# Kernel optimization log

Measured on AMD Instinct MI355X. Metric: run time of the kernel, lower is better.

## Reference

```python
import jax, jax.numpy as jnp
import numpy as np

M, K, D = 64, 32, 32   # antennas, users, hidden features
PT = 1.0               # total transmit power
BS = 1024


def _glorot(key, shape):
    fan_out, fan_in = shape
    lim = np.sqrt(6.0 / (fan_in + fan_out)).astype(np.float32)
    return jax.random.uniform(key, shape, minval=-lim, maxval=lim, dtype=jnp.float32)


def setup_inputs() -> dict:
    key = jax.random.key(0)
    ks = jax.random.split(key, 16)
    inp = {"x": jax.random.normal(ks[0], (BS, M, K, 2), dtype=jnp.float32)}
    dims = [(D, 2), (D, D), (D, D), (D, D), (2, D)]
    i = 1
    for l, sh in enumerate(dims, start=1):
        for tag in ("s", "m", "k"):
            inp[f"W{l}{tag}"] = _glorot(ks[i], sh)
            i += 1
    return inp


def gnn_layer(x, Ws, Wm, Wk):
    # x: (b, M, K, d_in); weights: (d_out, d_in)
    msg_m = jnp.sum(x, axis=2)  # (b, M, d_in) aggregate over users per antenna
    msg_k = jnp.sum(x, axis=1)  # (b, K, d_in) aggregate over antennas per user
    z = (jnp.einsum('hd,bmkd->bmkh', Ws, x)
         + jnp.einsum('hd,bmd->bmh', Wm, msg_m)[:, :, None, :]
         + jnp.einsum('hd,bkd->bkh', Wk, msg_k)[:, None, :, :])
    return z  # (b, M, K, d_out)


def pwr_norm(x):
    # x: (b, M, K, 2) -> |W|_F^2 = sum over m,k of re^2+im^2
    power = jnp.sum(x * x, axis=(1, 2, 3), keepdims=True)
    alpha = jnp.sqrt(PT / power)
    return alpha * x


def reference(x, W1s, W1m, W1k, W2s, W2m, W2k, W3s, W3m, W3k,
              W4s, W4m, W4k, W5s, W5m, W5k):
    h = jax.nn.relu(gnn_layer(x, W1s, W1m, W1k))
    h = jax.nn.relu(gnn_layer(h, W2s, W2m, W2k))
    h = jax.nn.relu(gnn_layer(h, W3s, W3m, W3k))
    h = jax.nn.relu(gnn_layer(h, W4s, W4m, W4k))
    h = gnn_layer(h, W5s, W5m, W5k)
    return pwr_norm(h)
```

## Files before the change

kernel.cpp:

```cpp
#include <hip/hip_runtime.h>
#include <hip/hip_fp16.h>


namespace {

constexpr int NTHREADS = 1024;
constexpr float INPUT_SCALE = 0.0625f;
constexpr float LAYER_SCALE = 0.0078125f;

typedef _Float16 half8 __attribute__((ext_vector_type(8)));
typedef _Float16 half2v __attribute__((ext_vector_type(2)));
typedef float    f32x4 __attribute__((ext_vector_type(4)));
typedef unsigned uint4v __attribute__((ext_vector_type(4)));

#define RPT32(X) X(0)X(1)X(2)X(3)X(4)X(5)X(6)X(7)X(8)X(9)X(10)X(11)X(12)X(13)X(14)X(15) \
                 X(16)X(17)X(18)X(19)X(20)X(21)X(22)X(23)X(24)X(25)X(26)X(27)X(28)X(29)X(30)X(31)
#define RPT16P(X) X(0,0,1)X(1,2,3)X(2,4,5)X(3,6,7)X(4,8,9)X(5,10,11)X(6,12,13)X(7,14,15) \
                  X(8,16,17)X(9,18,19)X(10,20,21)X(11,22,23)X(12,24,25)X(13,26,27)X(14,28,29)X(15,30,31)

#define AB_OFF(h) ((((h) >> 2) & 3) * 8 + (((h) >> 4) & 1) * 4 + ((h) & 3))
#define PSLOT(s) (2 * ((s) >> 2) + 8 * (((s) >> 1) & 1) + ((s) & 1))

__device__ __forceinline__ float2 upk(unsigned w) {
    __half2 h;
    *reinterpret_cast<unsigned*>(&h) = w;
    return __half22float2(h);
}
__device__ __forceinline__ unsigned pkz(float a, float b) {
    auto h = __builtin_amdgcn_cvt_pkrtz(a, b);
    return __builtin_bit_cast(unsigned, h);
}
__device__ __forceinline__ unsigned hadd2u(unsigned a, unsigned b) {
    half2v x = __builtin_bit_cast(half2v, a);
    half2v y = __builtin_bit_cast(half2v, b);
    return __builtin_bit_cast(unsigned, x + y);
}
__device__ __forceinline__ unsigned hmax0u(unsigned a) {
    unsigned r;
    asm("v_pk_max_f16 %0, %1, 0" : "=v"(r) : "v"(a));
    return r;
}
template <int CTRL>
__device__ __forceinline__ uint4v dpp_hadd(uint4v s) {
    uint4v r;
    r.x = hadd2u(s.x, (unsigned)__builtin_amdgcn_mov_dpp((int)s.x, CTRL, 0xF, 0xF, true));
    r.y = hadd2u(s.y, (unsigned)__builtin_amdgcn_mov_dpp((int)s.y, CTRL, 0xF, 0xF, true));
    r.z = hadd2u(s.z, (unsigned)__builtin_amdgcn_mov_dpp((int)s.z, CTRL, 0xF, 0xF, true));
    r.w = hadd2u(s.w, (unsigned)__builtin_amdgcn_mov_dpp((int)s.w, CTRL, 0xF, 0xF, true));
    return r;
}

__device__ __forceinline__ half8 load_wfrag(const float* __restrict__ W, int h, int quad,
                                            float scale) {
    const float4 w0 = *reinterpret_cast<const float4*>(W + h * 32 + quad * 4);
    const float4 w1 = *reinterpret_cast<const float4*>(W + h * 32 + 16 + quad * 4);
    half8 b;
    b[0] = (_Float16)(w0.x * scale); b[1] = (_Float16)(w0.y * scale);
    b[2] = (_Float16)(w0.z * scale); b[3] = (_Float16)(w0.w * scale);
    b[4] = (_Float16)(w1.x * scale); b[5] = (_Float16)(w1.y * scale);
    b[6] = (_Float16)(w1.z * scale); b[7] = (_Float16)(w1.w * scale);
    return b;
}

__device__ __forceinline__ void phase_msg(const unsigned* __restrict__ Xs,
                                          unsigned* __restrict__ MSG, int t) {
    const int l = t & 63, w = t >> 6;
    {
        const int k3 = l & 7;
        const int k = ((w & 3) << 3) | k3;
        const int chunk = w >> 2;
        const int mo = l >> 3;
        const int chunkp = chunk ^ ((k3 >> 1) & 3);
        const unsigned* p = Xs + mo * 4096 + k * 16 + chunkp * 4;
        half8 acc{};
#pragma unroll
        for (int j = 0; j < 8; ++j)
            acc += __builtin_bit_cast(half8, *(const uint4v*)(p + j * 512));
        uint4v s = __builtin_bit_cast(uint4v, acc);
        s = dpp_hadd<0x128>(s);
        if ((l & 8) == 0) {
            const int qi = l >> 4;
            *(uint4v*)(MSG + (128 + qi * 32 + k) * 20 + chunk * 4) = s;
        }
    }
    {
        const int k3 = l & 7;
        const int chunk = (l >> 3) & 3;
        const int mlow = ((l >> 5) & 1) | ((w & 15) << 1);
        const int chunkp = chunk ^ ((k3 >> 1) & 3);
        const unsigned* p = Xs + mlow * 512 + k3 * 16 + chunkp * 4;
        half8 accA{}, accB{};
#pragma unroll
        for (int j = 0; j < 4; ++j) {
            accA += __builtin_bit_cast(half8, *(const uint4v*)(p + j * 128));
            accB += __builtin_bit_cast(half8, *(const uint4v*)(p + 16384 + j * 128));
        }
        uint4v sA = __builtin_bit_cast(uint4v, accA);
        uint4v sB = __builtin_bit_cast(uint4v, accB);
        sA = dpp_hadd<0xB1>(sA); sA = dpp_hadd<0x4E>(sA);
        sB = dpp_hadd<0xB1>(sB); sB = dpp_hadd<0x4E>(sB);
        if ((l & 3) == 0) {
            const int set = (l >> 2) & 1;
            *(uint4v*)(MSG + (mlow + set * 64) * 20 + chunk * 4) = sA;
            *(uint4v*)(MSG + (mlow + 32 + set * 64) * 20 + chunk * 4) = sB;
        }
    }
}

__device__ __forceinline__ void phase_small(const float* __restrict__ Wmg,
                                            const float* __restrict__ Wkg,
                                            const unsigned* __restrict__ MSG,
                                            unsigned* __restrict__ ABu, int t) {
    const int w = t >> 6, lane = t & 63;
    if (w < 12) {
        const int isb = (w >= 8);
        const int ww = isb ? (w - 8) : w;
        const int nt = ww >> 1, ht = ww & 1;
        const int quad = lane >> 4, col = lane & 15;
        const half8 afrag = load_wfrag(isb ? Wkg : Wmg, ht * 16 + col, quad, LAYER_SCALE);
        f32x4 c = {0.f, 0.f, 0.f, 0.f};
        if (isb) {
            const int r0 = 128 + nt * 16 + col;
#pragma unroll
            for (int s = 0; s < 4; ++s) {
                const half8 bf = __builtin_bit_cast(half8,
                    *(const uint4v*)(MSG + (r0 + s * 32) * 20 + quad * 4));
                c = __builtin_amdgcn_mfma_f32_16x16x32_f16(afrag, bf, c, 0, 0, 0);
            }
        } else {
            const int r0 = nt * 16 + col;
#pragma unroll
            for (int s = 0; s < 2; ++s) {
                const half8 bf = __builtin_bit_cast(half8,
                    *(const uint4v*)(MSG + (r0 + s * 64) * 20 + quad * 4));
                c = __builtin_amdgcn_mfma_f32_16x16x32_f16(afrag, bf, c, 0, 0, 0);
            }
        }
        uint2 st;
        st.x = pkz(c[0], c[1]);
        st.y = pkz(c[2], c[3]);
        const int abrow = (isb ? 64 : 0) + nt * 16 + col;
        *reinterpret_cast<uint2*>(ABu + abrow * 20 + quad * 4 + ht * 2) = st;
    }
}

__device__ __forceinline__ void phase_main(const float* __restrict__ Wsg,
                                           unsigned* __restrict__ Xs,
                                           const unsigned* __restrict__ ABu, int t) {
    const int w = t >> 6, lane = t & 63;
    const int quad = lane >> 4, col = lane & 15;
    const half8 a0 = load_wfrag(Wsg, col, quad, LAYER_SCALE);
    const half8 a1 = load_wfrag(Wsg, 16 + col, quad, LAYER_SCALE);
    const uint4v* AB4 = reinterpret_cast<const uint4v*>(ABu);
    unsigned* xp = Xs + col * 16 + ((quad ^ ((col >> 1) & 3)) << 2);
#pragma unroll 2
    for (int i = 0; i < 8; ++i) {
        const int T = w + i * 16;
        const int m = T >> 1;
        const int k0 = (T & 1) << 4;
        unsigned* xc = xp + T * 256;
        const half8 b = __builtin_bit_cast(half8, *(const uint4v*)xc);
        const int krow = 64 + k0 + col;
        const uint4v Am = AB4[m * 5 + quad];
        const uint4v Bk = AB4[krow * 5 + quad];
        const float2 p00 = upk(hadd2u(Am.x, Bk.x));
        const float2 p01 = upk(hadd2u(Am.y, Bk.y));
        const float2 p10 = upk(hadd2u(Am.z, Bk.z));
        const float2 p11 = upk(hadd2u(Am.w, Bk.w));
        f32x4 c0 = {p00.x, p00.y, p01.x, p01.y};
        f32x4 c1 = {p10.x, p10.y, p11.x, p11.y};
        c0 = __builtin_amdgcn_mfma_f32_16x16x32_f16(a0, b, c0, 0, 0, 0);
        c1 = __builtin_amdgcn_mfma_f32_16x16x32_f16(a1, b, c1, 0, 0, 0);
        uint4v st;
        st.x = hmax0u(pkz(c0[0], c0[1]));
        st.y = hmax0u(pkz(c0[2], c0[3]));
        st.z = hmax0u(pkz(c1[0], c1[1]));
        st.w = hmax0u(pkz(c1[2], c1[3]));
        *(uint4v*)xc = st;
    }
}

__global__ void __launch_bounds__(NTHREADS) gnn_fused(
    const float* __restrict__ xg,
    const float* __restrict__ w1s, const float* __restrict__ w1m, const float* __restrict__ w1k,
    const float* __restrict__ w2s, const float* __restrict__ w2m, const float* __restrict__ w2k,
    const float* __restrict__ w3s, const float* __restrict__ w3m, const float* __restrict__ w3k,
    const float* __restrict__ w4s, const float* __restrict__ w4m, const float* __restrict__ w4k,
    const float* __restrict__ w5s, const float* __restrict__ w5m, const float* __restrict__ w5k,
    float* __restrict__ out)
{
    __shared__ __align__(16) unsigned Xs[2048 * 16];
    __shared__ __align__(16) unsigned MSG[256 * 20];
    __shared__ __align__(16) unsigned ABu[96 * 20];
    __shared__ float red[17];

    const int t = threadIdx.x;
    const int b = blockIdx.x;
    const int k = t & 31;
    const int m1 = t >> 5;
    const int m2 = m1 + 32;
    const int lane = t & 63;
    const int wave = t >> 6;
    const int sw1 = (t >> 1) & 3;

    float2 a1 = *reinterpret_cast<const float2*>(xg + (size_t)b * 4096 + 2 * t);
    float2 a2 = *reinterpret_cast<const float2*>(xg + (size_t)b * 4096 + 2048 + 2 * t);
    a1.x *= INPUT_SCALE; a1.y *= INPUT_SCALE;
    a2.x *= INPUT_SCALE; a2.y *= INPUT_SCALE;

    _Float16* ABf = reinterpret_cast<_Float16*>(ABu);
    float* MSGf = reinterpret_cast<float*>(MSG);

    if (t < 64) MSGf[t] = 0.f;
    __syncthreads();
    {
        float s0 = a1.x + a2.x, s1 = a1.y + a2.y;
        s0 += __shfl_xor(s0, 32);
        s1 += __shfl_xor(s1, 32);
        if (lane < 32) {
            atomicAdd(&MSGf[2 * k], s0);
            atomicAdd(&MSGf[2 * k + 1], s1);
        }
        float f0 = a1.x, f1 = a1.y, g0 = a2.x, g1 = a2.y;
#pragma unroll
        for (int mask = 1; mask <= 16; mask <<= 1) {
            f0 += __shfl_xor(f0, mask); f1 += __shfl_xor(f1, mask);
            g0 += __shfl_xor(g0, mask); g1 += __shfl_xor(g1, mask);
        }
        const float2 wm = *reinterpret_cast<const float2*>(w1m + 2 * k);
        ABf[m1 * 40 + AB_OFF(k)] = (_Float16)(wm.x * f0 + wm.y * f1);
        ABf[m2 * 40 + AB_OFF(k)] = (_Float16)(wm.x * g0 + wm.y * g1);
    }
    __syncthreads();
    {
        const int kk = t >> 5, hh = t & 31;
        const float2 wk2 = *reinterpret_cast<const float2*>(w1k + 2 * hh);
        ABf[(64 + kk) * 40 + AB_OFF(hh)] =
            (_Float16)(wk2.x * MSGf[2 * kk] + wk2.y * MSGf[2 * kk + 1]);
    }
    __syncthreads();
#pragma unroll 1
    for (int hf = 0; hf < 2; ++hf) {
        const int n = hf ? (t + 1024) : t;
        const int m = hf ? m2 : m1;
        const float xa = hf ? a2.x : a1.x;
        const float xb = hf ? a2.y : a1.y;
#define DECL_ACC(h) float acc##h = (float)ABf[m * 40 + AB_OFF(h)] \
                                 + (float)ABf[(64 + k) * 40 + AB_OFF(h)] \
                                 + w1s[h * 2] * xa + w1s[h * 2 + 1] * xb;
        RPT32(DECL_ACC)
#undef DECL_ACC
        unsigned tmp[16];
#define ST(p, h0, h1) tmp[p] = pkz(fmaxf(acc##h0, 0.f) * LAYER_SCALE, \
                                   fmaxf(acc##h1, 0.f) * LAYER_SCALE);
        RPT16P(ST)
#undef ST
        unsigned* xd = Xs + n * 16;
        uint4v v0, v1, v2, v3;
        v0.x = tmp[0]; v0.y = tmp[1]; v0.z = tmp[8];  v0.w = tmp[9];
        v1.x = tmp[2]; v1.y = tmp[3]; v1.z = tmp[10]; v1.w = tmp[11];
        v2.x = tmp[4]; v2.y = tmp[5]; v2.z = tmp[12]; v2.w = tmp[13];
        v3.x = tmp[6]; v3.y = tmp[7]; v3.z = tmp[14]; v3.w = tmp[15];
        *(uint4v*)(xd + ((0 ^ sw1) << 2)) = v0;
        *(uint4v*)(xd + ((1 ^ sw1) << 2)) = v1;
        *(uint4v*)(xd + ((2 ^ sw1) << 2)) = v2;
        *(uint4v*)(xd + ((3 ^ sw1) << 2)) = v3;
    }
    __syncthreads();

    phase_msg(Xs, MSG, t); __syncthreads();
    phase_small(w2m, w2k, MSG, ABu, t); __syncthreads();
    phase_main(w2s, Xs, ABu, t); __syncthreads();

    phase_msg(Xs, MSG, t); __syncthreads();
    phase_small(w3m, w3k, MSG, ABu, t); __syncthreads();
    phase_main(w3s, Xs, ABu, t); __syncthreads();

    phase_msg(Xs, MSG, t); __syncthreads();
    phase_small(w4m, w4k, MSG, ABu, t); __syncthreads();
    phase_main(w4s, Xs, ABu, t); __syncthreads();

    phase_msg(Xs, MSG, t); __syncthreads();
    if (t < 128) {
        const int m = t & 63, h = t >> 6;
        float acc = 0.f;
#pragma unroll
        for (int s = 0; s < 16; ++s) {
            const int pp = PSLOT(s);
            const float2 uA = upk(MSG[m * 20 + s]);
            const float2 uB = upk(MSG[(64 + m) * 20 + s]);
            acc += w5m[h * 32 + 2 * pp] * (uA.x + uB.x)
                 + w5m[h * 32 + 2 * pp + 1] * (uA.y + uB.y);
        }
        ABf[m * 40 + h] = (_Float16)acc;
    } else if (t < 192) {
        const int idx = t - 128;
        const int kk = idx & 31, h = idx >> 5;
        float acc = 0.f;
#pragma unroll
        for (int s = 0; s < 16; ++s) {
            const int pp = PSLOT(s);
            float ux = 0.f, uy = 0.f;
#pragma unroll
            for (int qq = 0; qq < 4; ++qq) {
                const float2 u = upk(MSG[(128 + qq * 32 + kk) * 20 + s]);
                ux += u.x; uy += u.y;
            }
            acc += w5k[h * 32 + 2 * pp] * ux + w5k[h * 32 + 2 * pp + 1] * uy;
        }
        ABf[(64 + kk) * 40 + h] = (_Float16)acc;
    }
    __syncthreads();

    float za0 = (float)ABf[m1 * 40 + 0] + (float)ABf[(64 + k) * 40 + 0];
    float za1 = (float)ABf[m1 * 40 + 1] + (float)ABf[(64 + k) * 40 + 1];
    float zb0 = (float)ABf[m2 * 40 + 0] + (float)ABf[(64 + k) * 40 + 0];
    float zb1 = (float)ABf[m2 * 40 + 1] + (float)ABf[(64 + k) * 40 + 1];
    {
        const unsigned* xa0 = Xs + t * 16;
        const unsigned* xb0 = xa0 + 16384;
#pragma unroll
        for (int s = 0; s < 16; ++s) {
            const int idx = ((((s >> 2) ^ sw1) << 2)) | (s & 3);
            const int pp = PSLOT(s);
            const float2 u = upk(xa0[idx]);
            za0 += w5s[2 * pp] * u.x + w5s[2 * pp + 1] * u.y;
            za1 += w5s[32 + 2 * pp] * u.x + w5s[32 + 2 * pp + 1] * u.y;
            const float2 v = upk(xb0[idx]);
            zb0 += w5s[2 * pp] * v.x + w5s[2 * pp + 1] * v.y;
            zb1 += w5s[32 + 2 * pp] * v.x + w5s[32 + 2 * pp + 1] * v.y;
        }
    }

    float p2 = za0 * za0 + za1 * za1 + zb0 * zb0 + zb1 * zb1;
#pragma unroll
    for (int mask = 1; mask <= 32; mask <<= 1) p2 += __shfl_xor(p2, mask);
    if (lane == 0) red[wave] = p2;
    __syncthreads();
    if (t == 0) {
        float tot = 0.f;
#pragma unroll
        for (int i = 0; i < 16; ++i) tot += red[i];
        red[16] = rsqrtf(tot);
    }
    __syncthreads();
    const float alpha = red[16];

    float2 r1, r2;
    r1.x = alpha * za0; r1.y = alpha * za1;
    r2.x = alpha * zb0; r2.y = alpha * zb1;
    *reinterpret_cast<float2*>(out + (size_t)b * 4096 + 2 * t) = r1;
    *reinterpret_cast<float2*>(out + (size_t)b * 4096 + 2048 + 2 * t) = r2;
}

}

extern "C" void kernel_launch(void* const* d_in, const int* in_sizes, int n_in,
                              void* d_out, int out_size, void* d_ws, size_t ws_size,
                              hipStream_t stream) {
    const float* xg  = (const float*)d_in[0];
    const float* w1s = (const float*)d_in[1];
    const float* w1m = (const float*)d_in[2];
    const float* w1k = (const float*)d_in[3];
    const float* w2s = (const float*)d_in[4];
    const float* w2m = (const float*)d_in[5];
    const float* w2k = (const float*)d_in[6];
    const float* w3s = (const float*)d_in[7];
    const float* w3m = (const float*)d_in[8];
    const float* w3k = (const float*)d_in[9];
    const float* w4s = (const float*)d_in[10];
    const float* w4m = (const float*)d_in[11];
    const float* w4k = (const float*)d_in[12];
    const float* w5s = (const float*)d_in[13];
    const float* w5m = (const float*)d_in[14];
    const float* w5k = (const float*)d_in[15];
    float* out = (float*)d_out;

    hipLaunchKernelGGL(gnn_fused, dim3(1024), dim3(NTHREADS), 0, stream,
                       xg, w1s, w1m, w1k, w2s, w2m, w2k, w3s, w3m, w3k,
                       w4s, w4m, w4k, w5s, w5m, w5k, out);
}
```

Measured before the change: 203.4 us.

## Fuse per-user message reduction into main GEMM epilogue with swizzled message buffers

The per-user (sum over antennas) message is now accumulated in registers inside phase_main as each output tile is written, and stored as 8 partial sets into a new swizzled MSGK buffer. This removes the separate shared-memory reduction pass over Xs for that message in layers 3–5, leaving only the per-antenna reduction. phase_small sums the partial sets via extra MFMA steps, and the final layer's user-message projection is spread over more threads with shuffle reductions and rotated reads to limit bank conflicts. Shared-memory layout changes to XOR-swizzled rows, and the loop unroll rises from 2 to 4.

```diff
diff --git a/kernel.cpp b/kernel.cpp
--- a/kernel.cpp
+++ b/kernel.cpp
@@ -20,6 +20,13 @@
 
 #define AB_OFF(h) ((((h) >> 2) & 3) * 8 + (((h) >> 4) & 1) * 4 + ((h) & 3))
 #define PSLOT(s) (2 * ((s) >> 2) + 8 * (((s) >> 1) & 1) + ((s) & 1))
+
+__device__ __forceinline__ int msgk_off(int set, int k, int chunk) {
+    return set * 512 + k * 16 + ((chunk ^ ((k >> 1) & 3)) << 2);
+}
+__device__ __forceinline__ int msgm_off(int row, int chunk) {
+    return row * 16 + ((chunk ^ ((row >> 1) & 3)) << 2);
+}
 
 __device__ __forceinline__ float2 upk(unsigned w) {
     __half2 h;
@@ -62,54 +69,57 @@
     return b;
 }
 
-__device__ __forceinline__ void phase_msg(const unsigned* __restrict__ Xs,
-                                          unsigned* __restrict__ MSG, int t) {
+__device__ __forceinline__ void phase_msgm(const unsigned* __restrict__ Xs,
+                                           unsigned* __restrict__ MSGM, int t) {
     const int l = t & 63, w = t >> 6;
-    {
-        const int k3 = l & 7;
-        const int k = ((w & 3) << 3) | k3;
-        const int chunk = w >> 2;
-        const int mo = l >> 3;
-        const int chunkp = chunk ^ ((k3 >> 1) & 3);
-        const unsigned* p = Xs + mo * 4096 + k * 16 + chunkp * 4;
-        half8 acc{};
-#pragma unroll
-        for (int j = 0; j < 8; ++j)
-            acc += __builtin_bit_cast(half8, *(const uint4v*)(p + j * 512));
-        uint4v s = __builtin_bit_cast(uint4v, acc);
-        s = dpp_hadd<0x128>(s);
-        if ((l & 8) == 0) {
-            const int qi = l >> 4;
-            *(uint4v*)(MSG + (128 + qi * 32 + k) * 20 + chunk * 4) = s;
-        }
-    }
-    {
-        const int k3 = l & 7;
-        const int chunk = (l >> 3) & 3;
-        const int mlow = ((l >> 5) & 1) | ((w & 15) << 1);
-        const int chunkp = chunk ^ ((k3 >> 1) & 3);
-        const unsigned* p = Xs + mlow * 512 + k3 * 16 + chunkp * 4;
-        half8 accA{}, accB{};
-#pragma unroll
-        for (int j = 0; j < 4; ++j) {
-            accA += __builtin_bit_cast(half8, *(const uint4v*)(p + j * 128));
-            accB += __builtin_bit_cast(half8, *(const uint4v*)(p + 16384 + j * 128));
-        }
-        uint4v sA = __builtin_bit_cast(uint4v, accA);
-        uint4v sB = __builtin_bit_cast(uint4v, accB);
-        sA = dpp_hadd<0xB1>(sA); sA = dpp_hadd<0x4E>(sA);
-        sB = dpp_hadd<0xB1>(sB); sB = dpp_hadd<0x4E>(sB);
-        if ((l & 3) == 0) {
-            const int set = (l >> 2) & 1;
-            *(uint4v*)(MSG + (mlow + set * 64) * 20 + chunk * 4) = sA;
-            *(uint4v*)(MSG + (mlow + 32 + set * 64) * 20 + chunk * 4) = sB;
-        }
-    }
-}
-
+    const int k3 = l & 7;
+    const int chunk = (l >> 3) & 3;
+    const int mlow = ((l >> 5) & 1) | ((w & 15) << 1);
+    const int chunkp = chunk ^ ((k3 >> 1) & 3);
+    const unsigned* p = Xs + mlow * 512 + k3 * 16 + chunkp * 4;
+    half8 accA{}, accB{};
+#pragma unroll
+    for (int j = 0; j < 4; ++j) {
+        accA += __builtin_bit_cast(half8, *(const uint4v*)(p + j * 128));
+        accB += __builtin_bit_cast(half8, *(const uint4v*)(p + 16384 + j * 128));
+    }
+    uint4v sA = __builtin_bit_cast(uint4v, accA);
+    uint4v sB = __builtin_bit_cast(uint4v, accB);
+    sA = dpp_hadd<0xB1>(sA); sA = dpp_hadd<0x4E>(sA);
+    sB = dpp_hadd<0xB1>(sB); sB = dpp_hadd<0x4E>(sB);
+    if ((l & 3) == 0) {
+        const int set = (l >> 2) & 1;
+        *(uint4v*)(MSGM + msgm_off(mlow + set * 64, chunk)) = sA;
+        *(uint4v*)(MSGM + msgm_off(mlow + 32 + set * 64, chunk)) = sB;
+    }
+}
+
+__device__ __forceinline__ void phase_msgk2(const unsigned* __restrict__ Xs,
+                                            unsigned* __restrict__ MSGK, int t) {
+    const int l = t & 63, w = t >> 6;
+    const int k3 = l & 7;
+    const int k = ((w & 3) << 3) | k3;
+    const int chunk = w >> 2;
+    const int mo = l >> 3;
+    const int chunkp = chunk ^ ((k3 >> 1) & 3);
+    const unsigned* p = Xs + mo * 4096 + k * 16 + chunkp * 4;
+    half8 acc{};
+#pragma unroll
+    for (int j = 0; j < 8; ++j)
+        acc += __builtin_bit_cast(half8, *(const uint4v*)(p + j * 512));
+    uint4v s = __builtin_bit_cast(uint4v, acc);
+    s = dpp_hadd<0x128>(s);
+    if ((l & 8) == 0) {
+        const int qi = l >> 4;
+        *(uint4v*)(MSGK + msgk_off(qi, k, chunk)) = s;
+    }
+}
+
+template <int NSETS>
 __device__ __forceinline__ void phase_small(const float* __restrict__ Wmg,
                                             const float* __restrict__ Wkg,
-                                            const unsigned* __restrict__ MSG,
+                                            const unsigned* __restrict__ MSGM,
+                                            const unsigned* __restrict__ MSGK,
                                             unsigned* __restrict__ ABu, int t) {
     const int w = t >> 6, lane = t & 63;
     if (w < 12) {
@@ -120,11 +130,11 @@
         const half8 afrag = load_wfrag(isb ? Wkg : Wmg, ht * 16 + col, quad, LAYER_SCALE);
         f32x4 c = {0.f, 0.f, 0.f, 0.f};
         if (isb) {
-            const int r0 = 128 + nt * 16 + col;
-#pragma unroll
-            for (int s = 0; s < 4; ++s) {
-                const half8 bf = __builtin_bit_cast(half8,
-                    *(const uint4v*)(MSG + (r0 + s * 32) * 20 + quad * 4));
+            const int kk = nt * 16 + col;
+            const unsigned* bp = MSGK + msgk_off(0, kk, quad);
+#pragma unroll
+            for (int s = 0; s < NSETS; ++s) {
+                const half8 bf = __builtin_bit_cast(half8, *(const uint4v*)(bp + s * 512));
                 c = __builtin_amdgcn_mfma_f32_16x16x32_f16(afrag, bf, c, 0, 0, 0);
             }
         } else {
@@ -132,7 +142,7 @@
 #pragma unroll
             for (int s = 0; s < 2; ++s) {
                 const half8 bf = __builtin_bit_cast(half8,
-                    *(const uint4v*)(MSG + (r0 + s * 64) * 20 + quad * 4));
+                    *(const uint4v*)(MSGM + msgm_off(r0 + s * 64, quad)));
                 c = __builtin_amdgcn_mfma_f32_16x16x32_f16(afrag, bf, c, 0, 0, 0);
             }
         }
@@ -146,14 +156,16 @@
 
 __device__ __forceinline__ void phase_main(const float* __restrict__ Wsg,
                                            unsigned* __restrict__ Xs,
-                                           const unsigned* __restrict__ ABu, int t) {
+                                           const unsigned* __restrict__ ABu,
+                                           unsigned* __restrict__ MSGK, int t) {
     const int w = t >> 6, lane = t & 63;
     const int quad = lane >> 4, col = lane & 15;
     const half8 a0 = load_wfrag(Wsg, col, quad, LAYER_SCALE);
     const half8 a1 = load_wfrag(Wsg, 16 + col, quad, LAYER_SCALE);
     const uint4v* AB4 = reinterpret_cast<const uint4v*>(ABu);
     unsigned* xp = Xs + col * 16 + ((quad ^ ((col >> 1) & 3)) << 2);
-#pragma unroll 2
+    uint4v msgp = {0u, 0u, 0u, 0u};
+#pragma unroll 4
     for (int i = 0; i < 8; ++i) {
         const int T = w + i * 16;
         const int m = T >> 1;
@@ -177,7 +189,14 @@
         st.z = hmax0u(pkz(c1[0], c1[1]));
         st.w = hmax0u(pkz(c1[2], c1[3]));
         *(uint4v*)xc = st;
-    }
+        msgp.x = hadd2u(msgp.x, st.x);
+        msgp.y = hadd2u(msgp.y, st.y);
+        msgp.z = hadd2u(msgp.z, st.z);
+        msgp.w = hadd2u(msgp.w, st.w);
+    }
+    const int set = w >> 1;
+    const int kk = ((w & 1) << 4) | col;
+    *(uint4v*)(MSGK + msgk_off(set, kk, quad)) = msgp;
 }
 
 __global__ void __launch_bounds__(NTHREADS) gnn_fused(
@@ -190,7 +209,8 @@
     float* __restrict__ out)
 {
     __shared__ __align__(16) unsigned Xs[2048 * 16];
-    __shared__ __align__(16) unsigned MSG[256 * 20];
+    __shared__ __align__(16) unsigned MSGK[8 * 512];
+    __shared__ __align__(16) unsigned MSGM[128 * 16];
     __shared__ __align__(16) unsigned ABu[96 * 20];
     __shared__ float red[17];
 
@@ -209,17 +229,17 @@
     a2.x *= INPUT_SCALE; a2.y *= INPUT_SCALE;
 
     _Float16* ABf = reinterpret_cast<_Float16*>(ABu);
-    float* MSGf = reinterpret_cast<float*>(MSG);
-
-    if (t < 64) MSGf[t] = 0.f;
+    float* MSGMf = reinterpret_cast<float*>(MSGM);
+
+    if (t < 64) MSGMf[t] = 0.f;
     __syncthreads();
     {
         float s0 = a1.x + a2.x, s1 = a1.y + a2.y;
         s0 += __shfl_xor(s0, 32);
         s1 += __shfl_xor(s1, 32);
         if (lane < 32) {
-            atomicAdd(&MSGf[2 * k], s0);
-            atomicAdd(&MSGf[2 * k + 1], s1);
+            atomicAdd(&MSGMf[2 * k], s0);
+            atomicAdd(&MSGMf[2 * k + 1], s1);
         }
         float f0 = a1.x, f1 = a1.y, g0 = a2.x, g1 = a2.y;
 #pragma unroll
@@ -236,7 +256,7 @@
         const int kk = t >> 5, hh = t & 31;
         const float2 wk2 = *reinterpret_cast<const float2*>(w1k + 2 * hh);
         ABf[(64 + kk) * 40 + AB_OFF(hh)] =
-            (_Float16)(wk2.x * MSGf[2 * kk] + wk2.y * MSGf[2 * kk + 1]);
+            (_Float16)(wk2.x * MSGMf[2 * kk] + wk2.y * MSGMf[2 * kk + 1]);
     }
     __syncthreads();
 #pragma unroll 1
@@ -268,47 +288,54 @@
     }
     __syncthreads();
 
-    phase_msg(Xs, MSG, t); __syncthreads();
-    phase_small(w2m, w2k, MSG, ABu, t); __syncthreads();
-    phase_main(w2s, Xs, ABu, t); __syncthreads();
-
-    phase_msg(Xs, MSG, t); __syncthreads();
-    phase_small(w3m, w3k, MSG, ABu, t); __syncthreads();
-    phase_main(w3s, Xs, ABu, t); __syncthreads();
-
-    phase_msg(Xs, MSG, t); __syncthreads();
-    phase_small(w4m, w4k, MSG, ABu, t); __syncthreads();
-    phase_main(w4s, Xs, ABu, t); __syncthreads();
-
-    phase_msg(Xs, MSG, t); __syncthreads();
+    phase_msgk2(Xs, MSGK, t);
+    phase_msgm(Xs, MSGM, t); __syncthreads();
+    phase_small<4>(w2m, w2k, MSGM, MSGK, ABu, t); __syncthreads();
+    phase_main(w2s, Xs, ABu, MSGK, t); __syncthreads();
+
+    phase_msgm(Xs, MSGM, t); __syncthreads();
+    phase_small<8>(w3m, w3k, MSGM, MSGK, ABu, t); __syncthreads();
+    phase_main(w3s, Xs, ABu, MSGK, t); __syncthreads();
+
+    phase_msgm(Xs, MSGM, t); __syncthreads();
+    phase_small<8>(w4m, w4k, MSGM, MSGK, ABu, t); __syncthreads();
+    phase_main(w4s, Xs, ABu, MSGK, t); __syncthreads();
+
+    phase_msgm(Xs, MSGM, t); __syncthreads();
     if (t < 128) {
         const int m = t & 63, h = t >> 6;
+        const int rot = (m >> 3) & 3;
         float acc = 0.f;
 #pragma unroll
-        for (int s = 0; s < 16; ++s) {
+        for (int s0 = 0; s0 < 16; ++s0) {
+            const int s = (s0 & 12) | ((s0 + rot) & 3);
             const int pp = PSLOT(s);
-            const float2 uA = upk(MSG[m * 20 + s]);
-            const float2 uB = upk(MSG[(64 + m) * 20 + s]);
+            const int idx = msgm_off(m, s >> 2) + (s & 3);
+            const float2 uA = upk(MSGM[idx]);
+            const float2 uB = upk(MSGM[idx + 1024]);
             acc += w5m[h * 32 + 2 * pp] * (uA.x + uB.x)
                  + w5m[h * 32 + 2 * pp + 1] * (uA.y + uB.y);
         }
         ABf[m * 40 + h] = (_Float16)acc;
-    } else if (t < 192) {
+    } else if (t < 384) {
         const int idx = t - 128;
-        const int kk = idx & 31, h = idx >> 5;
+        const int sp = idx & 3;
+        const int kk = (idx >> 2) & 31;
+        const int h = idx >> 7;
         float acc = 0.f;
 #pragma unroll
-        for (int s = 0; s < 16; ++s) {
+        for (int s0 = 0; s0 < 16; ++s0) {
+            const int s = (s0 & 12) | ((s0 + sp) & 3);
             const int pp = PSLOT(s);
-            float ux = 0.f, uy = 0.f;
-#pragma unroll
-            for (int qq = 0; qq < 4; ++qq) {
-                const float2 u = upk(MSG[(128 + qq * 32 + kk) * 20 + s]);
-                ux += u.x; uy += u.y;
-            }
-            acc += w5k[h * 32 + 2 * pp] * ux + w5k[h * 32 + 2 * pp + 1] * uy;
-        }
-        ABf[(64 + kk) * 40 + h] = (_Float16)acc;
+            const int off = msgk_off(0, kk, s >> 2) + (s & 3);
+            const float2 u0 = upk(MSGK[(2 * sp) * 512 + off]);
+            const float2 u1 = upk(MSGK[(2 * sp + 1) * 512 + off]);
+            acc += w5k[h * 32 + 2 * pp] * (u0.x + u1.x)
+                 + w5k[h * 32 + 2 * pp + 1] * (u0.y + u1.y);
+        }
+        acc += __shfl_xor(acc, 1);
+        acc += __shfl_xor(acc, 2);
+        if (sp == 0) ABf[(64 + kk) * 40 + h] = (_Float16)acc;
     }
     __syncthreads();
 
```

Result: no change. 201.1 us (-1.1%).
